# Optimization experiments

Hardware: AMD Instinct MI355X
Metric: run time of the kernel (lower is better)

## Reference

```python
import jax, jax.numpy as jnp
import numpy as np


def setup_inputs() -> dict:
    key = jax.random.key(0)
    k1, k2, k3, k4 = jax.random.split(key, 4)
    S, D, DKQ, DV = 8192, 2048, 128, 128
    x = jax.random.normal(k1, (S, D), dtype=jnp.float32)
    w_q = jax.random.uniform(k2, (D, DKQ), dtype=jnp.float32)
    w_k = jax.random.uniform(k3, (D, DKQ), dtype=jnp.float32)
    w_v = jax.random.uniform(k4, (D, DV), dtype=jnp.float32)
    return {"x": x, "w_q": w_q, "w_k": w_k, "w_v": w_v}


def reference(x, w_q, w_k, w_v):
    # x: [S, D]; single-head causal attention, unbatched as in the source.
    dim_kq = w_q.shape[1]
    q = x @ w_q  # [S, DKQ]
    k = x @ w_k  # [S, DKQ]
    v = x @ w_v  # [S, DV]
    scores = (q @ k.T) / jnp.sqrt(jnp.asarray(dim_kq, q.dtype))  # [S, S]
    S = scores.shape[0]
    causal = jnp.tril(jnp.ones((S, S), dtype=bool))
    scores = jnp.where(causal, scores, -jnp.inf)
    att_w = jax.nn.softmax(scores, axis=-1)
    return att_w @ v  # [S, DV]
```

## Files before the change

### kernel.cpp

```cpp
#include <hip/hip_runtime.h>

#define S_LEN 8192
#define D_DIM 2048
#define HD    128
#define KVB   32
#define NCH   8

typedef __attribute__((ext_vector_type(8))) short bf16x8;
typedef __attribute__((ext_vector_type(4))) float f32x4;

__device__ __forceinline__ unsigned short f2bf(float f) {
  unsigned int u = __float_as_uint(f);
  u += 0x7fffu + ((u >> 16) & 1u);
  return (unsigned short)(u >> 16);
}
__device__ __forceinline__ float bf2f(unsigned short h) {
  return __uint_as_float(((unsigned int)h) << 16);
}

__device__ __forceinline__ void glds16(const void* g, const short* l) {
  __builtin_amdgcn_global_load_lds(
      (const __attribute__((address_space(1))) void*)g,
      (__attribute__((address_space(3))) void*)l, 16, 0, 0);
}

__global__ __launch_bounds__(256)
void split_x_kernel(const float* __restrict__ x,
                    unsigned short* __restrict__ xh, unsigned short* __restrict__ xl)
{
  const size_t n4 = (size_t)S_LEN * D_DIM / 4;
  size_t idx = (size_t)blockIdx.x * 256 + threadIdx.x;
  const size_t stride = (size_t)gridDim.x * 256;
  for (; idx < n4; idx += stride) {
    float4 v = ((const float4*)x)[idx];
    ushort4 h, l;
#pragma unroll
    for (int j = 0; j < 4; ++j) {
      float f = ((const float*)&v)[j];
      unsigned short hb = f2bf(f);
      ((unsigned short*)&h)[j] = hb;
      ((unsigned short*)&l)[j] = f2bf(f - bf2f(hb));
    }
    ((ushort4*)xh)[idx] = h;
    ((ushort4*)xl)[idx] = l;
  }
}

__global__ __launch_bounds__(256)
void split_w_kernel(const float* __restrict__ wq, const float* __restrict__ wk,
                    const float* __restrict__ wv,
                    unsigned short* __restrict__ wTh, unsigned short* __restrict__ wTl)
{
  const int mode = blockIdx.y;
  const float* __restrict__ w = (mode == 0) ? wq : (mode == 1) ? wk : wv;
  unsigned short* __restrict__ oh = wTh + (size_t)mode * HD * D_DIM;
  unsigned short* __restrict__ ol = wTl + (size_t)mode * HD * D_DIM;
  const int k0 = blockIdx.x * 64;

  __shared__ float ws[64][132];
  const int t = threadIdx.x;
#pragma unroll
  for (int i = 0; i < 8; ++i) {
    int idx = t + i * 256;
    int row = idx >> 5;
    int c4  = idx & 31;
    *(float4*)&ws[row][c4 * 4] = *(const float4*)(w + (size_t)(k0 + row) * HD + c4 * 4);
  }
  __syncthreads();
#pragma unroll
  for (int i = 0; i < 4; ++i) {
    int task = t + i * 256;
    int col = task >> 3;
    int kc  = task & 7;
    ushort4 h[2], l[2];
#pragma unroll
    for (int e = 0; e < 8; ++e) {
      float f = ws[kc * 8 + e][col];
      unsigned short hb = f2bf(f);
      ((unsigned short*)&h[e >> 2])[e & 3] = hb;
      ((unsigned short*)&l[e >> 2])[e & 3] = f2bf(f - bf2f(hb));
    }
    size_t off = (size_t)col * D_DIM + k0 + kc * 8;
    *(ushort4*)(oh + off)     = h[0];
    *(ushort4*)(oh + off + 4) = h[1];
    *(ushort4*)(ol + off)     = l[0];
    *(ushort4*)(ol + off + 4) = l[1];
  }
}

__global__ __launch_bounds__(256)
void proj_kernel(const unsigned short* __restrict__ xh, const unsigned short* __restrict__ xl,
                 const unsigned short* __restrict__ wTh, const unsigned short* __restrict__ wTl,
                 unsigned short* __restrict__ q_hi, unsigned short* __restrict__ q_lo,
                 unsigned short* __restrict__ k_hi, unsigned short* __restrict__ k_lo,
                 unsigned short* __restrict__ vT)
{
  __shared__ short sm[2][12288];

  const int mode = blockIdx.y;
  const int mt   = blockIdx.x;
  const bool split = (mode < 2);

  const unsigned short* gxh = xh + (size_t)mt * 64 * D_DIM;
  const unsigned short* gxl = xl + (size_t)mt * 64 * D_DIM;
  const unsigned short* gwh = wTh + (size_t)mode * HD * D_DIM;
  const unsigned short* gwl = wTl + (size_t)mode * HD * D_DIM;

  const int t   = threadIdx.x;
  const int wid = t >> 6;
  const int ln  = t & 63;
  const int cl  = ln & 15;
  const int g4  = ln >> 4;

  auto stage = [&](int kt, int buf) {
    short* b = sm[buf];
    {
      int slot = wid * 64 + ln;
      int row = slot >> 2, sc = slot & 3;
      int kof = (sc ^ (row & 3)) * 8;
      glds16(gxh + (size_t)row * D_DIM + kt + kof, b + wid * 512);
      if (split)
        glds16(gxl + (size_t)row * D_DIM + kt + kof, b + 2048 + wid * 512);
    }
#pragma unroll
    for (int g = 0; g < 2; ++g) {
      int slot = g * 256 + wid * 64 + ln;
      int col = slot >> 2, sc = slot & 3;
      int kof = (sc ^ (col & 3)) * 8;
      glds16(gwh + (size_t)col * D_DIM + kt + kof, b + 4096 + (g * 256 + wid * 64) * 8);
      if (split)
        glds16(gwl + (size_t)col * D_DIM + kt + kof, b + 8192 + (g * 256 + wid * 64) * 8);
    }
  };

  f32x4 acc[2][4];
#pragma unroll
  for (int m = 0; m < 2; ++m)
#pragma unroll
    for (int n = 0; n < 4; ++n) acc[m][n] = f32x4{0.f, 0.f, 0.f, 0.f};

  stage(0, 0);
  __syncthreads();

  for (int kt = 0, step = 0; kt < D_DIM; kt += 32, ++step) {
    const int cur = step & 1;
    if (kt + 32 < D_DIM) stage(kt + 32, cur ^ 1);

    const short* b = sm[cur];
    bf16x8 a_h[2], a_l[2], b_h[4], b_l[4];
#pragma unroll
    for (int m = 0; m < 2; ++m) {
      int row = (wid >> 1) * 32 + m * 16 + cl;
      int byte = row * 64 + ((g4 ^ (row & 3)) << 4);
      a_h[m] = *(const bf16x8*)((const char*)b + byte);
      if (split) a_l[m] = *(const bf16x8*)((const char*)b + 4096 + byte);
    }
#pragma unroll
    for (int n = 0; n < 4; ++n) {
      int col = (wid & 1) * 64 + n * 16 + cl;
      int byte = col * 64 + ((g4 ^ (col & 3)) << 4);
      b_h[n] = *(const bf16x8*)((const char*)b + 8192 + byte);
      if (split) b_l[n] = *(const bf16x8*)((const char*)b + 16384 + byte);
    }

#pragma unroll
    for (int m = 0; m < 2; ++m)
#pragma unroll
      for (int n = 0; n < 4; ++n)
        acc[m][n] = __builtin_amdgcn_mfma_f32_16x16x32_bf16(a_h[m], b_h[n], acc[m][n], 0, 0, 0);
    if (split) {
#pragma unroll
      for (int m = 0; m < 2; ++m)
#pragma unroll
        for (int n = 0; n < 4; ++n) {
          acc[m][n] = __builtin_amdgcn_mfma_f32_16x16x32_bf16(a_l[m], b_h[n], acc[m][n], 0, 0, 0);
          acc[m][n] = __builtin_amdgcn_mfma_f32_16x16x32_bf16(a_h[m], b_l[n], acc[m][n], 0, 0, 0);
        }
    }
    __syncthreads();
  }

  const int rbase = mt * 64 + (wid >> 1) * 32 + g4 * 4;
  const int cbase = (wid & 1) * 64 + cl;

  if (mode < 2) {
    const float scale = (mode == 0) ? 0.08838834764831843f : 1.0f;
    unsigned short* __restrict__ oh = (mode == 0) ? q_hi : k_hi;
    unsigned short* __restrict__ ol = (mode == 0) ? q_lo : k_lo;
#pragma unroll
    for (int m = 0; m < 2; ++m)
#pragma unroll
      for (int n = 0; n < 4; ++n)
#pragma unroll
        for (int r = 0; r < 4; ++r) {
          float val = acc[m][n][r] * scale;
          unsigned short hb = f2bf(val);
          size_t off = (size_t)(rbase + m * 16 + r) * HD + cbase + n * 16;
          oh[off] = hb;
          ol[off] = f2bf(val - bf2f(hb));
        }
  } else {
#pragma unroll
    for (int m = 0; m < 2; ++m)
#pragma unroll
      for (int n = 0; n < 4; ++n) {
        ushort4 o;
#pragma unroll
        for (int r = 0; r < 4; ++r) ((unsigned short*)&o)[r] = f2bf(acc[m][n][r]);
        int col = cbase + n * 16;
        *(ushort4*)(vT + (size_t)col * S_LEN + rbase + m * 16) = o;
      }
  }
}

__global__ __launch_bounds__(256, 3)
void attn_kernel(const unsigned short* __restrict__ q_hi, const unsigned short* __restrict__ q_lo,
                 const unsigned short* __restrict__ k_hi, const unsigned short* __restrict__ k_lo,
                 const unsigned short* __restrict__ vT,
                 float* __restrict__ part_o, float* __restrict__ part_ml)
{
  __shared__ short ls_kh[2][4096];
  __shared__ short ls_kl[2][4096];
  __shared__ short ls_v [2][4096];
  __shared__ short ls_p [4][640];

  const int t   = threadIdx.x;
  const int wid = t >> 6;
  const int ln  = t & 63;
  const int cl  = ln & 15;
  const int g4  = ln >> 4;
  const int pairId = blockIdx.x >> 3;
  const int chunk  = blockIdx.x & 7;

  short* pw = ls_p[wid];

  auto stage = [&](int j, int buf) {
    const unsigned short* gkh = k_hi + (size_t)j * KVB * HD;
    const unsigned short* gkl = k_lo + (size_t)j * KVB * HD;
    const unsigned short* gv  = vT + (size_t)j * KVB;
#pragma unroll
    for (int i = 0; i < 2; ++i) {
      int slot = wid * 128 + i * 64 + ln;
      int row = slot >> 4, sc = slot & 15;
      int c16 = sc ^ (row & 7);
      glds16(gkh + row * HD + c16 * 8, &ls_kh[buf][(wid * 128 + i * 64) * 8]);
      glds16(gkl + row * HD + c16 * 8, &ls_kl[buf][(wid * 128 + i * 64) * 8]);
    }
#pragma unroll
    for (int i = 0; i < 2; ++i) {
      int slot = wid * 128 + i * 64 + ln;
      int d = slot >> 2, sub = slot & 3;
      int s2 = sub ^ ((d >> 1) & 3);
      glds16(gv + (size_t)d * S_LEN + s2 * 8, &ls_v[buf][(wid * 128 + i * 64) * 8]);
    }
  };

  for (int hh = 0; hh < 2; ++hh) {
    const int T = hh ? (127 - pairId) : pairId;
    const int jmaxB = T * 2 + 1;
    const int jmaxW = T * 2 + (wid >> 1);
    const int rowbase = T * 64 + wid * 16;

    bf16x8 qh[4], ql[4];
    {
      const size_t qoff = ((size_t)rowbase + cl) * HD + g4 * 8;
#pragma unroll
      for (int kc = 0; kc < 4; ++kc) {
        qh[kc] = *(const bf16x8*)(q_hi + qoff + kc * 32);
        ql[kc] = *(const bf16x8*)(q_lo + qoff + kc * 32);
      }
    }

    float m_i[4], l_i[4];
    f32x4 o_acc[8];
#pragma unroll
    for (int i = 0; i < 4; ++i) { m_i[i] = -1e30f; l_i[i] = 0.f; }
#pragma unroll
    for (int c = 0; c < 8; ++c) o_acc[c] = f32x4{0.f, 0.f, 0.f, 0.f};

    if (chunk <= jmaxB) {
      int cur = 0;
      stage(chunk, 0);
      __syncthreads();
      for (int j = chunk; j <= jmaxB; j += NCH) {
        if (j + NCH <= jmaxB) stage(j + NCH, cur ^ 1);

        if (j <= jmaxW) {
          f32x4 s[2];
          s[0] = f32x4{0.f, 0.f, 0.f, 0.f};
          s[1] = f32x4{0.f, 0.f, 0.f, 0.f};
#pragma unroll
          for (int kc = 0; kc < 4; ++kc) {
#pragma unroll
            for (int c = 0; c < 2; ++c) {
              const int kcol = c * 16 + cl;
              const int byte = kcol * 256 + ((((kc << 2) + g4) ^ (kcol & 7)) << 4);
              bf16x8 khf = *(const bf16x8*)((const char*)ls_kh[cur] + byte);
              bf16x8 klf = *(const bf16x8*)((const char*)ls_kl[cur] + byte);
              s[c] = __builtin_amdgcn_mfma_f32_16x16x32_bf16(qh[kc], khf, s[c], 0, 0, 0);
              s[c] = __builtin_amdgcn_mfma_f32_16x16x32_bf16(ql[kc], khf, s[c], 0, 0, 0);
              s[c] = __builtin_amdgcn_mfma_f32_16x16x32_bf16(qh[kc], klf, s[c], 0, 0, 0);
            }
          }

          if (j * KVB + KVB - 1 > rowbase) {
#pragma unroll
            for (int c = 0; c < 2; ++c)
#pragma unroll
              for (int i = 0; i < 4; ++i) {
                int col = j * KVB + c * 16 + cl;
                int row = rowbase + g4 * 4 + i;
                if (col > row) s[c][i] = -1e30f;
              }
          }

          bool ok = true;
#pragma unroll
          for (int i = 0; i < 4; ++i) {
            float mx = fmaxf(s[0][i], s[1][i]);
            ok = ok && (mx <= m_i[i] + 8.0f);
          }
          if (!__all(ok)) {
#pragma unroll
            for (int i = 0; i < 4; ++i) {
              float rm = fmaxf(s[0][i], s[1][i]);
              rm = fmaxf(rm, __shfl_xor(rm, 1));
              rm = fmaxf(rm, __shfl_xor(rm, 2));
              rm = fmaxf(rm, __shfl_xor(rm, 4));
              rm = fmaxf(rm, __shfl_xor(rm, 8));
              float mnew = fmaxf(m_i[i], rm);
              float corr = __expf(m_i[i] - mnew);
              l_i[i] *= corr;
#pragma unroll
              for (int c2 = 0; c2 < 8; ++c2) o_acc[c2][i] *= corr;
              m_i[i] = mnew;
            }
          }

#pragma unroll
          for (int c = 0; c < 2; ++c)
#pragma unroll
            for (int i = 0; i < 4; ++i) {
              float sv = s[c][i];
              float p = (sv > -1e29f) ? __expf(sv - m_i[i]) : 0.f;
              l_i[i] += p;
              pw[(g4 * 4 + i) * 40 + c * 16 + cl] = (short)f2bf(p);
            }

          bf16x8 pa = *(const bf16x8*)((const char*)pw + cl * 80 + g4 * 16);
#pragma unroll
          for (int c2 = 0; c2 < 8; ++c2) {
            const int d = c2 * 16 + cl;
            const int byte = d * 64 + (((g4 ^ ((d >> 1) & 3))) << 4);
            bf16x8 vb = *(const bf16x8*)((const char*)ls_v[cur] + byte);
            o_acc[c2] = __builtin_amdgcn_mfma_f32_16x16x32_bf16(pa, vb, o_acc[c2], 0, 0, 0);
          }
        }

        __syncthreads();
        cur ^= 1;
      }
    }

    const int base = T * NCH + chunk;
#pragma unroll
    for (int c2 = 0; c2 < 8; ++c2)
#pragma unroll
      for (int i = 0; i < 4; ++i)
        part_o[((size_t)base * 64 + wid * 16 + g4 * 4 + i) * HD + c2 * 16 + cl] = o_acc[c2][i];

#pragma unroll
    for (int i = 0; i < 4; ++i) {
      float lv = l_i[i];
      lv += __shfl_xor(lv, 1);
      lv += __shfl_xor(lv, 2);
      lv += __shfl_xor(lv, 4);
      lv += __shfl_xor(lv, 8);
      if (cl == 0) {
        int rl = wid * 16 + g4 * 4 + i;
        part_ml[base * 128 + rl]      = m_i[i];
        part_ml[base * 128 + 64 + rl] = lv;
      }
    }
  }
}

__global__ __launch_bounds__(128)
void merge_kernel(const float* __restrict__ part_o, const float* __restrict__ part_ml,
                  float* __restrict__ out)
{
  const int row = blockIdx.x;
  const int T   = row >> 6;
  const int r   = row & 63;
  const int c   = threadIdx.x;

  float m[NCH], l[NCH];
  float mstar = -3e38f;
#pragma unroll
  for (int s = 0; s < NCH; ++s) {
    m[s] = part_ml[(T * NCH + s) * 128 + r];
    l[s] = part_ml[(T * NCH + s) * 128 + 64 + r];
    mstar = fmaxf(mstar, m[s]);
  }
  float num = 0.f, den = 0.f;
#pragma unroll
  for (int s = 0; s < NCH; ++s) {
    float wgt = __expf(m[s] - mstar);
    den += l[s] * wgt;
    num += wgt * part_o[((size_t)(T * NCH + s) * 64 + r) * HD + c];
  }
  out[(size_t)row * HD + c] = num / den;
}

extern "C" void kernel_launch(void* const* d_in, const int* in_sizes, int n_in,
                              void* d_out, int out_size, void* d_ws, size_t ws_size,
                              hipStream_t stream)
{
  const float* x  = (const float*)d_in[0];
  const float* wq = (const float*)d_in[1];
  const float* wk = (const float*)d_in[2];
  const float* wv = (const float*)d_in[3];
  float* out = (float*)d_out;

  unsigned short* p = (unsigned short*)d_ws;
  unsigned short* xh = p;  p += (size_t)S_LEN * D_DIM;
  unsigned short* xl = p;  p += (size_t)S_LEN * D_DIM;
  unsigned short* wTh = p; p += (size_t)3 * HD * D_DIM;
  unsigned short* wTl = p; p += (size_t)3 * HD * D_DIM;
  unsigned short* q_hi = p; p += (size_t)S_LEN * HD;
  unsigned short* q_lo = p; p += (size_t)S_LEN * HD;
  unsigned short* k_hi = p; p += (size_t)S_LEN * HD;
  unsigned short* k_lo = p; p += (size_t)S_LEN * HD;
  unsigned short* vT   = p; p += (size_t)S_LEN * HD;
  float* part_o  = (float*)xh;
  float* part_ml = (float*)xl;

  split_x_kernel<<<4096, 256, 0, stream>>>(x, xh, xl);
  split_w_kernel<<<dim3(32, 3), 256, 0, stream>>>(wq, wk, wv, wTh, wTl);
  proj_kernel<<<dim3(128, 3), 256, 0, stream>>>(xh, xl, wTh, wTl,
                                                q_hi, q_lo, k_hi, k_lo, vT);
  attn_kernel<<<dim3(512), 256, 0, stream>>>(q_hi, q_lo, k_hi, k_lo, vT,
                                             part_o, part_ml);
  merge_kernel<<<dim3(8192), 128, 0, stream>>>(part_o, part_ml, out);
}
```

Measured before the change: 151.1 us.

## Fuse x split into projection, raise attention chunking, store partials as bf16

The standalone split_x pass is removed. The projection kernel now reads fp32 x directly, splits it into hi/lo bf16 in registers and writes it to LDS, using 32-row tiles and twice as many blocks. The attention kernel splits KV into 12 chunks instead of 8, wraps its MFMA blocks in s_setprio, and stores partial outputs as bf16 to halve merge traffic. This saves a full read/write of x and a launch, but the bf16 partials cost accuracy and the projection now reads x redundantly across the three modes.

```diff
diff --git a/kernel.cpp b/kernel.cpp
--- a/kernel.cpp
+++ b/kernel.cpp
@@ -4,7 +4,8 @@
 #define D_DIM 2048
 #define HD    128
 #define KVB   32
-#define NCH   8
+#define NCH   12
+#define NB    1536
 
 typedef __attribute__((ext_vector_type(8))) short bf16x8;
 typedef __attribute__((ext_vector_type(4))) float f32x4;
@@ -22,28 +23,6 @@
   __builtin_amdgcn_global_load_lds(
       (const __attribute__((address_space(1))) void*)g,
       (__attribute__((address_space(3))) void*)l, 16, 0, 0);
-}
-
-__global__ __launch_bounds__(256)
-void split_x_kernel(const float* __restrict__ x,
-                    unsigned short* __restrict__ xh, unsigned short* __restrict__ xl)
-{
-  const size_t n4 = (size_t)S_LEN * D_DIM / 4;
-  size_t idx = (size_t)blockIdx.x * 256 + threadIdx.x;
-  const size_t stride = (size_t)gridDim.x * 256;
-  for (; idx < n4; idx += stride) {
-    float4 v = ((const float4*)x)[idx];
-    ushort4 h, l;
-#pragma unroll
-    for (int j = 0; j < 4; ++j) {
-      float f = ((const float*)&v)[j];
-      unsigned short hb = f2bf(f);
-      ((unsigned short*)&h)[j] = hb;
-      ((unsigned short*)&l)[j] = f2bf(f - bf2f(hb));
-    }
-    ((ushort4*)xh)[idx] = h;
-    ((ushort4*)xl)[idx] = l;
-  }
 }
 
 __global__ __launch_bounds__(256)
@@ -89,20 +68,18 @@
 }
 
 __global__ __launch_bounds__(256)
-void proj_kernel(const unsigned short* __restrict__ xh, const unsigned short* __restrict__ xl,
+void proj_kernel(const float* __restrict__ x,
                  const unsigned short* __restrict__ wTh, const unsigned short* __restrict__ wTl,
                  unsigned short* __restrict__ q_hi, unsigned short* __restrict__ q_lo,
                  unsigned short* __restrict__ k_hi, unsigned short* __restrict__ k_lo,
                  unsigned short* __restrict__ vT)
 {
-  __shared__ short sm[2][12288];
+  __shared__ short sm[2][10240];
 
   const int mode = blockIdx.y;
   const int mt   = blockIdx.x;
   const bool split = (mode < 2);
 
-  const unsigned short* gxh = xh + (size_t)mt * 64 * D_DIM;
-  const unsigned short* gxl = xl + (size_t)mt * 64 * D_DIM;
   const unsigned short* gwh = wTh + (size_t)mode * HD * D_DIM;
   const unsigned short* gwl = wTl + (size_t)mode * HD * D_DIM;
 
@@ -112,75 +89,87 @@
   const int cl  = ln & 15;
   const int g4  = ln >> 4;
 
-  auto stage = [&](int kt, int buf) {
+  const int rowx = t >> 3, kqx = t & 7;
+  const float* gx = x + (size_t)(mt * 32 + rowx) * D_DIM + kqx * 4;
+  const int xdst = rowx * 32 + (((kqx >> 1) ^ (rowx & 3)) << 3) + (kqx & 1) * 4;
+
+  auto stagew = [&](int kt, int buf) {
     short* b = sm[buf];
-    {
-      int slot = wid * 64 + ln;
-      int row = slot >> 2, sc = slot & 3;
-      int kof = (sc ^ (row & 3)) * 8;
-      glds16(gxh + (size_t)row * D_DIM + kt + kof, b + wid * 512);
-      if (split)
-        glds16(gxl + (size_t)row * D_DIM + kt + kof, b + 2048 + wid * 512);
-    }
 #pragma unroll
     for (int g = 0; g < 2; ++g) {
-      int slot = g * 256 + wid * 64 + ln;
+      int slot = g * 256 + t;
       int col = slot >> 2, sc = slot & 3;
       int kof = (sc ^ (col & 3)) * 8;
-      glds16(gwh + (size_t)col * D_DIM + kt + kof, b + 4096 + (g * 256 + wid * 64) * 8);
+      glds16(gwh + (size_t)col * D_DIM + kt + kof, b + 2048 + slot * 8);
       if (split)
-        glds16(gwl + (size_t)col * D_DIM + kt + kof, b + 8192 + (g * 256 + wid * 64) * 8);
+        glds16(gwl + (size_t)col * D_DIM + kt + kof, b + 6144 + slot * 8);
     }
   };
-
-  f32x4 acc[2][4];
-#pragma unroll
-  for (int m = 0; m < 2; ++m)
-#pragma unroll
-    for (int n = 0; n < 4; ++n) acc[m][n] = f32x4{0.f, 0.f, 0.f, 0.f};
-
-  stage(0, 0);
+  auto writex = [&](const float4& a0, int buf) {
+    short* b = sm[buf];
+    ushort4 hv, lv;
+#pragma unroll
+    for (int e = 0; e < 4; ++e) {
+      float f = ((const float*)&a0)[e];
+      unsigned short hb = f2bf(f);
+      ((unsigned short*)&hv)[e] = hb;
+      ((unsigned short*)&lv)[e] = f2bf(f - bf2f(hb));
+    }
+    *(ushort4*)(b + xdst) = hv;
+    if (split) *(ushort4*)(b + 1024 + xdst) = lv;
+  };
+
+  f32x4 acc[4];
+#pragma unroll
+  for (int n = 0; n < 4; ++n) acc[n] = f32x4{0.f, 0.f, 0.f, 0.f};
+
+  {
+    float4 a0 = *(const float4*)gx;
+    stagew(0, 0);
+    writex(a0, 0);
+  }
   __syncthreads();
 
   for (int kt = 0, step = 0; kt < D_DIM; kt += 32, ++step) {
     const int cur = step & 1;
-    if (kt + 32 < D_DIM) stage(kt + 32, cur ^ 1);
+    const bool more = (kt + 32 < D_DIM);
+    float4 n0;
+    if (more) {
+      n0 = *(const float4*)(gx + kt + 32);
+      stagew(kt + 32, cur ^ 1);
+    }
 
     const short* b = sm[cur];
-    bf16x8 a_h[2], a_l[2], b_h[4], b_l[4];
-#pragma unroll
-    for (int m = 0; m < 2; ++m) {
-      int row = (wid >> 1) * 32 + m * 16 + cl;
-      int byte = row * 64 + ((g4 ^ (row & 3)) << 4);
-      a_h[m] = *(const bf16x8*)((const char*)b + byte);
-      if (split) a_l[m] = *(const bf16x8*)((const char*)b + 4096 + byte);
+    bf16x8 a_h, a_l, b_h[4], b_l[4];
+    {
+      int row = (wid >> 1) * 16 + cl;
+      int byteA = row * 64 + ((g4 ^ (row & 3)) << 4);
+      a_h = *(const bf16x8*)((const char*)b + byteA);
+      if (split) a_l = *(const bf16x8*)((const char*)b + 2048 + byteA);
     }
 #pragma unroll
     for (int n = 0; n < 4; ++n) {
       int col = (wid & 1) * 64 + n * 16 + cl;
-      int byte = col * 64 + ((g4 ^ (col & 3)) << 4);
-      b_h[n] = *(const bf16x8*)((const char*)b + 8192 + byte);
-      if (split) b_l[n] = *(const bf16x8*)((const char*)b + 16384 + byte);
-    }
-
-#pragma unroll
-    for (int m = 0; m < 2; ++m)
-#pragma unroll
-      for (int n = 0; n < 4; ++n)
-        acc[m][n] = __builtin_amdgcn_mfma_f32_16x16x32_bf16(a_h[m], b_h[n], acc[m][n], 0, 0, 0);
+      int byteB = col * 64 + ((g4 ^ (col & 3)) << 4);
+      b_h[n] = *(const bf16x8*)((const char*)b + 4096 + byteB);
+      if (split) b_l[n] = *(const bf16x8*)((const char*)b + 12288 + byteB);
+    }
+
+#pragma unroll
+    for (int n = 0; n < 4; ++n)
+      acc[n] = __builtin_amdgcn_mfma_f32_16x16x32_bf16(a_h, b_h[n], acc[n], 0, 0, 0);
     if (split) {
 #pragma unroll
-      for (int m = 0; m < 2; ++m)
-#pragma unroll
-        for (int n = 0; n < 4; ++n) {
-          acc[m][n] = __builtin_amdgcn_mfma_f32_16x16x32_bf16(a_l[m], b_h[n], acc[m][n], 0, 0, 0);
-          acc[m][n] = __builtin_amdgcn_mfma_f32_16x16x32_bf16(a_h[m], b_l[n], acc[m][n], 0, 0, 0);
-        }
-    }
+      for (int n = 0; n < 4; ++n) {
+        acc[n] = __builtin_amdgcn_mfma_f32_16x16x32_bf16(a_l, b_h[n], acc[n], 0, 0, 0);
+        acc[n] = __builtin_amdgcn_mfma_f32_16x16x32_bf16(a_h, b_l[n], acc[n], 0, 0, 0);
+      }
+    }
+    if (more) writex(n0, cur ^ 1);
     __syncthreads();
   }
 
-  const int rbase = mt * 64 + (wid >> 1) * 32 + g4 * 4;
+  const int rbase = mt * 32 + (wid >> 1) * 16 + g4 * 4;
   const int cbase = (wid & 1) * 64 + cl;
 
   if (mode < 2) {
@@ -188,28 +177,24 @@
     unsigned short* __restrict__ oh = (mode == 0) ? q_hi : k_hi;
     unsigned short* __restrict__ ol = (mode == 0) ? q_lo : k_lo;
 #pragma unroll
-    for (int m = 0; m < 2; ++m)
-#pragma unroll
-      for (int n = 0; n < 4; ++n)
-#pragma unroll
-        for (int r = 0; r < 4; ++r) {
-          float val = acc[m][n][r] * scale;
-          unsigned short hb = f2bf(val);
-          size_t off = (size_t)(rbase + m * 16 + r) * HD + cbase + n * 16;
-          oh[off] = hb;
-          ol[off] = f2bf(val - bf2f(hb));
-        }
+    for (int n = 0; n < 4; ++n)
+#pragma unroll
+      for (int r = 0; r < 4; ++r) {
+        float val = acc[n][r] * scale;
+        unsigned short hb = f2bf(val);
+        size_t off = (size_t)(rbase + r) * HD + cbase + n * 16;
+        oh[off] = hb;
+        ol[off] = f2bf(val - bf2f(hb));
+      }
   } else {
 #pragma unroll
-    for (int m = 0; m < 2; ++m)
-#pragma unroll
-      for (int n = 0; n < 4; ++n) {
-        ushort4 o;
-#pragma unroll
-        for (int r = 0; r < 4; ++r) ((unsigned short*)&o)[r] = f2bf(acc[m][n][r]);
-        int col = cbase + n * 16;
-        *(ushort4*)(vT + (size_t)col * S_LEN + rbase + m * 16) = o;
-      }
+    for (int n = 0; n < 4; ++n) {
+      ushort4 o;
+#pragma unroll
+      for (int r = 0; r < 4; ++r) ((unsigned short*)&o)[r] = f2bf(acc[n][r]);
+      int col = cbase + n * 16;
+      *(ushort4*)(vT + (size_t)col * S_LEN + rbase) = o;
+    }
   }
 }
 
@@ -217,7 +202,7 @@
 void attn_kernel(const unsigned short* __restrict__ q_hi, const unsigned short* __restrict__ q_lo,
                  const unsigned short* __restrict__ k_hi, const unsigned short* __restrict__ k_lo,
                  const unsigned short* __restrict__ vT,
-                 float* __restrict__ part_o, float* __restrict__ part_ml)
+                 unsigned short* __restrict__ part_o, float* __restrict__ part_ml)
 {
   __shared__ short ls_kh[2][4096];
   __shared__ short ls_kl[2][4096];
@@ -229,8 +214,8 @@
   const int ln  = t & 63;
   const int cl  = ln & 15;
   const int g4  = ln >> 4;
-  const int pairId = blockIdx.x >> 3;
-  const int chunk  = blockIdx.x & 7;
+  const int pairId = blockIdx.x / NCH;
+  const int chunk  = blockIdx.x % NCH;
 
   short* pw = ls_p[wid];
 
@@ -289,6 +274,7 @@
           f32x4 s[2];
           s[0] = f32x4{0.f, 0.f, 0.f, 0.f};
           s[1] = f32x4{0.f, 0.f, 0.f, 0.f};
+          __builtin_amdgcn_s_setprio(1);
 #pragma unroll
           for (int kc = 0; kc < 4; ++kc) {
 #pragma unroll
@@ -302,6 +288,7 @@
               s[c] = __builtin_amdgcn_mfma_f32_16x16x32_bf16(qh[kc], klf, s[c], 0, 0, 0);
             }
           }
+          __builtin_amdgcn_s_setprio(0);
 
           if (j * KVB + KVB - 1 > rowbase) {
 #pragma unroll
@@ -348,6 +335,7 @@
             }
 
           bf16x8 pa = *(const bf16x8*)((const char*)pw + cl * 80 + g4 * 16);
+          __builtin_amdgcn_s_setprio(1);
 #pragma unroll
           for (int c2 = 0; c2 < 8; ++c2) {
             const int d = c2 * 16 + cl;
@@ -355,6 +343,7 @@
             bf16x8 vb = *(const bf16x8*)((const char*)ls_v[cur] + byte);
             o_acc[c2] = __builtin_amdgcn_mfma_f32_16x16x32_bf16(pa, vb, o_acc[c2], 0, 0, 0);
           }
+          __builtin_amdgcn_s_setprio(0);
         }
 
         __syncthreads();
@@ -367,7 +356,8 @@
     for (int c2 = 0; c2 < 8; ++c2)
 #pragma unroll
       for (int i = 0; i < 4; ++i)
-        part_o[((size_t)base * 64 + wid * 16 + g4 * 4 + i) * HD + c2 * 16 + cl] = o_acc[c2][i];
+        part_o[((size_t)base * 64 + wid * 16 + g4 * 4 + i) * HD + c2 * 16 + cl] =
+            f2bf(o_acc[c2][i]);
 
 #pragma unroll
     for (int i = 0; i < 4; ++i) {
@@ -386,7 +376,7 @@
 }
 
 __global__ __launch_bounds__(128)
-void merge_kernel(const float* __restrict__ part_o, const float* __restrict__ part_ml,
+void merge_kernel(const unsigned short* __restrict__ part_o, const float* __restrict__ part_ml,
                   float* __restrict__ out)
 {
   const int row = blockIdx.x;
@@ -407,7 +397,7 @@
   for (int s = 0; s < NCH; ++s) {
     float wgt = __expf(m[s] - mstar);
     den += l[s] * wgt;
-    num += wgt * part_o[((size_t)(T * NCH + s) * 64 + r) * HD + c];
+    num += wgt * bf2f(part_o[((size_t)(T * NCH + s) * 64 + r) * HD + c]);
   }
   out[(size_t)row * HD + c] = num / den;
 }
@@ -432,14 +422,13 @@
   unsigned short* k_hi = p; p += (size_t)S_LEN * HD;
   unsigned short* k_lo = p; p += (size_t)S_LEN * HD;
   unsigned short* vT   = p; p += (size_t)S_LEN * HD;
-  float* part_o  = (float*)xh;
-  float* part_ml = (float*)xl;
-
-  split_x_kernel<<<4096, 256, 0, stream>>>(x, xh, xl);
+  unsigned short* part_o = xh;
+  float* part_ml = (float*)wTh;
+
   split_w_kernel<<<dim3(32, 3), 256, 0, stream>>>(wq, wk, wv, wTh, wTl);
-  proj_kernel<<<dim3(128, 3), 256, 0, stream>>>(xh, xl, wTh, wTl,
+  proj_kernel<<<dim3(256, 3), 256, 0, stream>>>(x, wTh, wTl,
                                                 q_hi, q_lo, k_hi, k_lo, vT);
-  attn_kernel<<<dim3(512), 256, 0, stream>>>(q_hi, q_lo, k_hi, k_lo, vT,
-                                             part_o, part_ml);
+  attn_kernel<<<dim3(64 * NCH), 256, 0, stream>>>(q_hi, q_lo, k_hi, k_lo, vT,
+                                                  part_o, part_ml);
   merge_kernel<<<dim3(8192), 128, 0, stream>>>(part_o, part_ml, out);
 }
```

Measured after the change: 160.1 us. +5.9%, slower.

## Fuse x splitting into projection, widen attention tiles, bf16 partials, setprio

Applied to the files above, without the earlier changes.

Removes the separate split_x pass: the projection kernel now reads fp32 x directly, splits it into hi/lo bf16 in registers and writes the parts to LDS. This avoids a full write and re-read of the split x buffers. The attention kernel moves to 512-thread blocks covering 128-row tiles with 16 KV chunks. It stores partial outputs as bf16, simplifies the causal mask test, and raises wave priority around the MFMA sections. The merge kernel is adapted to the new layout. Storing partials in bf16 lowers their precision, and the larger blocks may reduce occupancy.

```diff
diff --git a/kernel.cpp b/kernel.cpp
--- a/kernel.cpp
+++ b/kernel.cpp
@@ -4,7 +4,7 @@
 #define D_DIM 2048
 #define HD    128
 #define KVB   32
-#define NCH   8
+#define NCH   16
 
 typedef __attribute__((ext_vector_type(8))) short bf16x8;
 typedef __attribute__((ext_vector_type(4))) float f32x4;
@@ -22,28 +22,6 @@
   __builtin_amdgcn_global_load_lds(
       (const __attribute__((address_space(1))) void*)g,
       (__attribute__((address_space(3))) void*)l, 16, 0, 0);
-}
-
-__global__ __launch_bounds__(256)
-void split_x_kernel(const float* __restrict__ x,
-                    unsigned short* __restrict__ xh, unsigned short* __restrict__ xl)
-{
-  const size_t n4 = (size_t)S_LEN * D_DIM / 4;
-  size_t idx = (size_t)blockIdx.x * 256 + threadIdx.x;
-  const size_t stride = (size_t)gridDim.x * 256;
-  for (; idx < n4; idx += stride) {
-    float4 v = ((const float4*)x)[idx];
-    ushort4 h, l;
-#pragma unroll
-    for (int j = 0; j < 4; ++j) {
-      float f = ((const float*)&v)[j];
-      unsigned short hb = f2bf(f);
-      ((unsigned short*)&h)[j] = hb;
-      ((unsigned short*)&l)[j] = f2bf(f - bf2f(hb));
-    }
-    ((ushort4*)xh)[idx] = h;
-    ((ushort4*)xl)[idx] = l;
-  }
 }
 
 __global__ __launch_bounds__(256)
@@ -89,7 +67,7 @@
 }
 
 __global__ __launch_bounds__(256)
-void proj_kernel(const unsigned short* __restrict__ xh, const unsigned short* __restrict__ xl,
+void proj_kernel(const float* __restrict__ x,
                  const unsigned short* __restrict__ wTh, const unsigned short* __restrict__ wTl,
                  unsigned short* __restrict__ q_hi, unsigned short* __restrict__ q_lo,
                  unsigned short* __restrict__ k_hi, unsigned short* __restrict__ k_lo,
@@ -101,8 +79,6 @@
   const int mt   = blockIdx.x;
   const bool split = (mode < 2);
 
-  const unsigned short* gxh = xh + (size_t)mt * 64 * D_DIM;
-  const unsigned short* gxl = xl + (size_t)mt * 64 * D_DIM;
   const unsigned short* gwh = wTh + (size_t)mode * HD * D_DIM;
   const unsigned short* gwl = wTl + (size_t)mode * HD * D_DIM;
 
@@ -112,16 +88,13 @@
   const int cl  = ln & 15;
   const int g4  = ln >> 4;
 
-  auto stage = [&](int kt, int buf) {
+  const int slotx = wid * 64 + ln;
+  const int rowx  = slotx >> 2, scx = slotx & 3;
+  const int kofx  = (scx ^ (rowx & 3)) * 8;
+  const float* gx = x + (size_t)(mt * 64 + rowx) * D_DIM + kofx;
+
+  auto stagew = [&](int kt, int buf) {
     short* b = sm[buf];
-    {
-      int slot = wid * 64 + ln;
-      int row = slot >> 2, sc = slot & 3;
-      int kof = (sc ^ (row & 3)) * 8;
-      glds16(gxh + (size_t)row * D_DIM + kt + kof, b + wid * 512);
-      if (split)
-        glds16(gxl + (size_t)row * D_DIM + kt + kof, b + 2048 + wid * 512);
-    }
 #pragma unroll
     for (int g = 0; g < 2; ++g) {
       int slot = g * 256 + wid * 64 + ln;
@@ -132,6 +105,21 @@
         glds16(gwl + (size_t)col * D_DIM + kt + kof, b + 8192 + (g * 256 + wid * 64) * 8);
     }
   };
+  auto writex = [&](const float4& a0, const float4& a1, int buf) {
+    short* b = sm[buf];
+    float fv[8];
+    *(float4*)&fv[0] = a0;
+    *(float4*)&fv[4] = a1;
+    bf16x8 hv, lv;
+#pragma unroll
+    for (int e = 0; e < 8; ++e) {
+      unsigned short hb = f2bf(fv[e]);
+      hv[e] = (short)hb;
+      lv[e] = (short)f2bf(fv[e] - bf2f(hb));
+    }
+    *(bf16x8*)(b + slotx * 8) = hv;
+    if (split) *(bf16x8*)(b + 2048 + slotx * 8) = lv;
+  };
 
   f32x4 acc[2][4];
 #pragma unroll
@@ -139,12 +127,23 @@
 #pragma unroll
     for (int n = 0; n < 4; ++n) acc[m][n] = f32x4{0.f, 0.f, 0.f, 0.f};
 
-  stage(0, 0);
+  {
+    float4 a0 = *(const float4*)(gx + 0);
+    float4 a1 = *(const float4*)(gx + 4);
+    stagew(0, 0);
+    writex(a0, a1, 0);
+  }
   __syncthreads();
 
   for (int kt = 0, step = 0; kt < D_DIM; kt += 32, ++step) {
     const int cur = step & 1;
-    if (kt + 32 < D_DIM) stage(kt + 32, cur ^ 1);
+    const bool more = (kt + 32 < D_DIM);
+    float4 n0, n1;
+    if (more) {
+      n0 = *(const float4*)(gx + kt + 32);
+      n1 = *(const float4*)(gx + kt + 36);
+      stagew(kt + 32, cur ^ 1);
+    }
 
     const short* b = sm[cur];
     bf16x8 a_h[2], a_l[2], b_h[4], b_l[4];
@@ -177,6 +176,7 @@
           acc[m][n] = __builtin_amdgcn_mfma_f32_16x16x32_bf16(a_h[m], b_l[n], acc[m][n], 0, 0, 0);
         }
     }
+    if (more) writex(n0, n1, cur ^ 1);
     __syncthreads();
   }
 
@@ -213,24 +213,24 @@
   }
 }
 
-__global__ __launch_bounds__(256, 3)
+__global__ __launch_bounds__(512)
 void attn_kernel(const unsigned short* __restrict__ q_hi, const unsigned short* __restrict__ q_lo,
                  const unsigned short* __restrict__ k_hi, const unsigned short* __restrict__ k_lo,
                  const unsigned short* __restrict__ vT,
-                 float* __restrict__ part_o, float* __restrict__ part_ml)
+                 unsigned short* __restrict__ part_o, float* __restrict__ part_ml)
 {
   __shared__ short ls_kh[2][4096];
   __shared__ short ls_kl[2][4096];
   __shared__ short ls_v [2][4096];
-  __shared__ short ls_p [4][640];
+  __shared__ short ls_p [8][640];
 
   const int t   = threadIdx.x;
   const int wid = t >> 6;
   const int ln  = t & 63;
   const int cl  = ln & 15;
   const int g4  = ln >> 4;
-  const int pairId = blockIdx.x >> 3;
-  const int chunk  = blockIdx.x & 7;
+  const int pairId = blockIdx.x >> 4;
+  const int chunk  = blockIdx.x & 15;
 
   short* pw = ls_p[wid];
 
@@ -238,28 +238,24 @@
     const unsigned short* gkh = k_hi + (size_t)j * KVB * HD;
     const unsigned short* gkl = k_lo + (size_t)j * KVB * HD;
     const unsigned short* gv  = vT + (size_t)j * KVB;
-#pragma unroll
-    for (int i = 0; i < 2; ++i) {
-      int slot = wid * 128 + i * 64 + ln;
-      int row = slot >> 4, sc = slot & 15;
+    {
+      int row = t >> 4, sc = t & 15;
       int c16 = sc ^ (row & 7);
-      glds16(gkh + row * HD + c16 * 8, &ls_kh[buf][(wid * 128 + i * 64) * 8]);
-      glds16(gkl + row * HD + c16 * 8, &ls_kl[buf][(wid * 128 + i * 64) * 8]);
-    }
-#pragma unroll
-    for (int i = 0; i < 2; ++i) {
-      int slot = wid * 128 + i * 64 + ln;
-      int d = slot >> 2, sub = slot & 3;
+      glds16(gkh + row * HD + c16 * 8, &ls_kh[buf][t * 8]);
+      glds16(gkl + row * HD + c16 * 8, &ls_kl[buf][t * 8]);
+    }
+    {
+      int d = t >> 2, sub = t & 3;
       int s2 = sub ^ ((d >> 1) & 3);
-      glds16(gv + (size_t)d * S_LEN + s2 * 8, &ls_v[buf][(wid * 128 + i * 64) * 8]);
+      glds16(gv + (size_t)d * S_LEN + s2 * 8, &ls_v[buf][t * 8]);
     }
   };
 
   for (int hh = 0; hh < 2; ++hh) {
-    const int T = hh ? (127 - pairId) : pairId;
-    const int jmaxB = T * 2 + 1;
-    const int jmaxW = T * 2 + (wid >> 1);
-    const int rowbase = T * 64 + wid * 16;
+    const int T = hh ? (63 - pairId) : pairId;
+    const int jmaxB = 4 * T + 3;
+    const int jmaxW = 4 * T + (wid >> 1);
+    const int rowbase = T * 128 + wid * 16;
 
     bf16x8 qh[4], ql[4];
     {
@@ -289,6 +285,7 @@
           f32x4 s[2];
           s[0] = f32x4{0.f, 0.f, 0.f, 0.f};
           s[1] = f32x4{0.f, 0.f, 0.f, 0.f};
+          __builtin_amdgcn_s_setprio(1);
 #pragma unroll
           for (int kc = 0; kc < 4; ++kc) {
 #pragma unroll
@@ -302,8 +299,9 @@
               s[c] = __builtin_amdgcn_mfma_f32_16x16x32_bf16(qh[kc], klf, s[c], 0, 0, 0);
             }
           }
-
-          if (j * KVB + KVB - 1 > rowbase) {
+          __builtin_amdgcn_s_setprio(0);
+
+          if (j == jmaxW) {
 #pragma unroll
             for (int c = 0; c < 2; ++c)
 #pragma unroll
@@ -348,6 +346,7 @@
             }
 
           bf16x8 pa = *(const bf16x8*)((const char*)pw + cl * 80 + g4 * 16);
+          __builtin_amdgcn_s_setprio(1);
 #pragma unroll
           for (int c2 = 0; c2 < 8; ++c2) {
             const int d = c2 * 16 + cl;
@@ -355,6 +354,7 @@
             bf16x8 vb = *(const bf16x8*)((const char*)ls_v[cur] + byte);
             o_acc[c2] = __builtin_amdgcn_mfma_f32_16x16x32_bf16(pa, vb, o_acc[c2], 0, 0, 0);
           }
+          __builtin_amdgcn_s_setprio(0);
         }
 
         __syncthreads();
@@ -366,8 +366,10 @@
 #pragma unroll
     for (int c2 = 0; c2 < 8; ++c2)
 #pragma unroll
-      for (int i = 0; i < 4; ++i)
-        part_o[((size_t)base * 64 + wid * 16 + g4 * 4 + i) * HD + c2 * 16 + cl] = o_acc[c2][i];
+      for (int i = 0; i < 4; ++i) {
+        int row = wid * 16 + g4 * 4 + i;
+        part_o[((size_t)base * 128 + row) * HD + c2 * 16 + cl] = f2bf(o_acc[c2][i]);
+      }
 
 #pragma unroll
     for (int i = 0; i < 4; ++i) {
@@ -377,29 +379,29 @@
       lv += __shfl_xor(lv, 4);
       lv += __shfl_xor(lv, 8);
       if (cl == 0) {
-        int rl = wid * 16 + g4 * 4 + i;
-        part_ml[base * 128 + rl]      = m_i[i];
-        part_ml[base * 128 + 64 + rl] = lv;
+        int row = wid * 16 + g4 * 4 + i;
+        part_ml[base * 256 + row]       = m_i[i];
+        part_ml[base * 256 + 128 + row] = lv;
       }
     }
   }
 }
 
 __global__ __launch_bounds__(128)
-void merge_kernel(const float* __restrict__ part_o, const float* __restrict__ part_ml,
+void merge_kernel(const unsigned short* __restrict__ part_o, const float* __restrict__ part_ml,
                   float* __restrict__ out)
 {
   const int row = blockIdx.x;
-  const int T   = row >> 6;
-  const int r   = row & 63;
+  const int T   = row >> 7;
+  const int r   = row & 127;
   const int c   = threadIdx.x;
 
   float m[NCH], l[NCH];
   float mstar = -3e38f;
 #pragma unroll
   for (int s = 0; s < NCH; ++s) {
-    m[s] = part_ml[(T * NCH + s) * 128 + r];
-    l[s] = part_ml[(T * NCH + s) * 128 + 64 + r];
+    m[s] = part_ml[(T * NCH + s) * 256 + r];
+    l[s] = part_ml[(T * NCH + s) * 256 + 128 + r];
     mstar = fmaxf(mstar, m[s]);
   }
   float num = 0.f, den = 0.f;
@@ -407,7 +409,7 @@
   for (int s = 0; s < NCH; ++s) {
     float wgt = __expf(m[s] - mstar);
     den += l[s] * wgt;
-    num += wgt * part_o[((size_t)(T * NCH + s) * 64 + r) * HD + c];
+    num += wgt * bf2f(part_o[((size_t)(T * NCH + s) * 128 + r) * HD + c]);
   }
   out[(size_t)row * HD + c] = num / den;
 }
@@ -432,14 +434,13 @@
   unsigned short* k_hi = p; p += (size_t)S_LEN * HD;
   unsigned short* k_lo = p; p += (size_t)S_LEN * HD;
   unsigned short* vT   = p; p += (size_t)S_LEN * HD;
-  float* part_o  = (float*)xh;
-  float* part_ml = (float*)xl;
-
-  split_x_kernel<<<4096, 256, 0, stream>>>(x, xh, xl);
+  unsigned short* part_o = xh;
+  float* part_ml = (float*)wTh;
+
   split_w_kernel<<<dim3(32, 3), 256, 0, stream>>>(wq, wk, wv, wTh, wTl);
-  proj_kernel<<<dim3(128, 3), 256, 0, stream>>>(xh, xl, wTh, wTl,
+  proj_kernel<<<dim3(128, 3), 256, 0, stream>>>(x, wTh, wTl,
                                                 q_hi, q_lo, k_hi, k_lo, vT);
-  attn_kernel<<<dim3(512), 256, 0, stream>>>(q_hi, q_lo, k_hi, k_lo, vT,
+  attn_kernel<<<dim3(512), 512, 0, stream>>>(q_hi, q_lo, k_hi, k_lo, vT,
                                              part_o, part_ml);
   merge_kernel<<<dim3(8192), 128, 0, stream>>>(part_o, part_ml, out);
 }
```

Result: no change. 149.6 us (-1.0%).
